# Optimization experiments

Hardware: AMD Instinct MI355X
Metric: run time of the kernel (lower is better)

The kernel has to match this reference:

```python
import jax, jax.numpy as jnp
import numpy as np
from jax import lax

HEADS = 4
SR = 4
LN_EPS = 1e-5


def setup_inputs() -> dict:
    key = jax.random.key(0)
    ks = jax.random.split(key, 8)
    B, N, C = 8, 4096, 256
    w_scale = 0.05  # keep attention logits in a sane range
    return {
        "x": jax.random.normal(ks[0], (B, N, C), jnp.float32),
        "h": 64,
        "w": 64,
        "Wq": jax.random.normal(ks[1], (C, C), jnp.float32) * w_scale,
        "Wkv": jax.random.normal(ks[2], (C, 2 * C), jnp.float32) * w_scale,
        "sr_w": jax.random.normal(ks[3], (C, C, SR, SR), jnp.float32) * w_scale,
        "sr_b": jnp.zeros((C,), jnp.float32),
        "ln_g": jnp.ones((C,), jnp.float32),
        "ln_b": jnp.zeros((C,), jnp.float32),
        "Wo": jax.random.normal(ks[4], (C, C), jnp.float32) * w_scale,
        "bo": jnp.zeros((C,), jnp.float32),
    }


def _layernorm(x, g, b):
    mu = x.mean(-1, keepdims=True)
    var = ((x - mu) ** 2).mean(-1, keepdims=True)
    return (x - mu) * lax.rsqrt(var + LN_EPS) * g + b


def reference(x, h, w, Wq, Wkv, sr_w, sr_b, ln_g, ln_b, Wo, bo):
    B, N, C = x.shape
    hd = C // HEADS
    scale = hd ** -0.5
    # Q projection -> [B, H, N, hd]
    q = (x @ Wq).reshape(B, N, HEADS, hd).transpose(0, 2, 1, 3)
    # spatial reduction of K/V tokens: strided conv + LayerNorm
    x_kv = x.transpose(0, 2, 1).reshape(B, C, h, w)  # b (h w) c -> b c h w
    x_kv = lax.conv_general_dilated(
        x_kv, sr_w, window_strides=(SR, SR), padding="VALID",
        dimension_numbers=("NCHW", "OIHW", "NCHW"))
    x_kv = x_kv + sr_b[None, :, None, None]
    Nk = (h // SR) * (w // SR)
    x_kv = x_kv.reshape(B, C, Nk).transpose(0, 2, 1)  # b c h w -> b (h w) c
    x_kv = _layernorm(x_kv, ln_g, ln_b)
    # KV projection -> k, v each [B, H, Nk, hd]
    kv = (x_kv @ Wkv).reshape(B, Nk, 2, HEADS, hd)
    k = kv[:, :, 0].transpose(0, 2, 1, 3)
    v = kv[:, :, 1].transpose(0, 2, 1, 3)
    # attention: full [B, H, N, Nk] score matrix, softmax over kv axis
    att = jax.nn.softmax(jnp.einsum("bhxd,bhyd->bhxy", q, k) * scale, axis=-1)
    out = jnp.einsum("bhxy,bhyd->bhxd", att, v)
    out = out.transpose(0, 2, 1, 3).reshape(B, N, C)  # b h l d -> b l (h d)
    return out @ Wo + bo
```

## Files before the change

kernel.cpp:

```cpp
#include <hip/hip_runtime.h>

typedef __bf16 bf16;
typedef bf16 bf16x8 __attribute__((ext_vector_type(8)));
typedef bf16 bf16x4 __attribute__((ext_vector_type(4)));
typedef float f32x4 __attribute__((ext_vector_type(4)));

#define MFMA16(a, b, c) __builtin_amdgcn_mfma_f32_16x16x32_bf16(a, b, c, 0, 0, 0)

__global__ void k_prep(const float* __restrict__ x, const float* __restrict__ Wq,
                       const float* __restrict__ Wkv, const float* __restrict__ Wo,
                       const float* __restrict__ srw,
                       bf16* __restrict__ x_bf, bf16* __restrict__ WqT,
                       bf16* __restrict__ WkvT, bf16* __restrict__ WoT,
                       bf16* __restrict__ srwT) {
  int bid = blockIdx.x, tid = threadIdx.x;
  if (bid < 8192) {
    int i = (bid * 256 + tid) * 4;
    float4 v = *(const float4*)(x + i);
    bf16x4 o;
    o[0] = (bf16)v.x; o[1] = (bf16)v.y; o[2] = (bf16)v.z; o[3] = (bf16)v.w;
    *(bf16x4*)(x_bf + i) = o;
  } else if (bid < 9216) {
    int id = (bid - 8192) * 256 + tid;
    if (id < 65536) {
      int c = id >> 8, r = id & 255;
      WqT[id] = (bf16)Wq[r * 256 + c];
    } else if (id < 196608) {
      int l = id - 65536;
      int c = l >> 8, r = l & 255;
      WkvT[l] = (bf16)Wkv[r * 512 + c];
    } else {
      int l = id - 196608;
      int c = l >> 8, r = l & 255;
      WoT[l] = (bf16)Wo[r * 256 + c];
    }
  } else {
    int id4 = ((bid - 9216) * 256 + tid) * 4;
    int o = id4 >> 12, rem = id4 & 4095;
    int i = rem >> 4, p = rem & 15;
    float4 v = *(const float4*)(srw + id4);
    srwT[(o << 12) + ((p + 0) << 8) + i] = (bf16)v.x;
    srwT[(o << 12) + ((p + 1) << 8) + i] = (bf16)v.y;
    srwT[(o << 12) + ((p + 2) << 8) + i] = (bf16)v.z;
    srwT[(o << 12) + ((p + 3) << 8) + i] = (bf16)v.w;
  }
}

template <int AMODE, int EMODE>
__global__ __launch_bounds__(256, 2) void k_gemm(
    const bf16* __restrict__ A, const bf16* __restrict__ Bt,
    void* __restrict__ Cout, const float* __restrict__ bias,
    int M, int N, int K) {
  constexpr int LDT = 72;
  __shared__ alignas(16) bf16 As[64 * LDT];
  __shared__ alignas(16) bf16 Bs[64 * LDT];
  int tid = threadIdx.x;
  int m0 = blockIdx.x * 64, n0 = blockIdx.y * 64;
  int kbeg = blockIdx.z * K;
  int wave = tid >> 6, lane = tid & 63;
  int quad = lane >> 4, l16 = lane & 15;

  f32x4 acc[4];
#pragma unroll
  for (int i = 0; i < 4; i++) acc[i] = (f32x4){0.f, 0.f, 0.f, 0.f};

  for (int k0 = kbeg; k0 < kbeg + K; k0 += 64) {
#pragma unroll
    for (int t = 0; t < 2; t++) {
      int c = tid + t * 256;
      int row = c >> 3, c8 = (c & 7) * 8;
      const bf16* asrc;
      if constexpr (AMODE == 0) {
        asrc = A + (size_t)(m0 + row) * K + k0 + c8;
      } else {
        int m = m0 + row;
        int b = m >> 8, tt = m & 255;
        int oh = tt >> 4, ow = tt & 15;
        int p = k0 >> 8;
        int kh = p >> 2, kw = p & 3;
        int tok = (oh * 4 + kh) * 64 + ow * 4 + kw;
        asrc = A + ((size_t)(b * 4096 + tok) << 8) + (k0 & 255) + c8;
      }
      *(bf16x8*)&As[row * LDT + c8] = *(const bf16x8*)asrc;
      *(bf16x8*)&Bs[row * LDT + c8] =
          *(const bf16x8*)(Bt + (size_t)(n0 + row) * ((AMODE == 1) ? 4096 : K) + k0 + c8);
    }
    __syncthreads();
#pragma unroll
    for (int kk = 0; kk < 64; kk += 32) {
      bf16x8 af = *(const bf16x8*)&As[(wave * 16 + l16) * LDT + kk + quad * 8];
#pragma unroll
      for (int nt = 0; nt < 4; nt++) {
        bf16x8 bfr = *(const bf16x8*)&Bs[(nt * 16 + l16) * LDT + kk + quad * 8];
        acc[nt] = MFMA16(af, bfr, acc[nt]);
      }
    }
    __syncthreads();
  }

  int rbase = m0 + wave * 16 + quad * 4;
#pragma unroll
  for (int nt = 0; nt < 4; nt++) {
    int col = n0 + nt * 16 + l16;
#pragma unroll
    for (int r = 0; r < 4; r++) {
      float v = acc[nt][r];
      int row = rbase + r;
      if constexpr (EMODE == 2) {
        int b = row >> 8, key = row & 255;
        int isv = col >> 8, c2 = col & 255;
        int hh = c2 >> 6, d = c2 & 63;
        int bh = b * 4 + hh;
        bf16* dst = (bf16*)Cout;
        if (isv == 0)
          dst[(((size_t)bh) * 256 + key) * 64 + d] = (bf16)v;
        else
          dst[32 * 256 * 64 + (((size_t)bh) * 64 + d) * 256 + key] = (bf16)v;
      } else if constexpr (EMODE == 3) {
        ((float*)Cout)[(size_t)row * N + col] = v + bias[col];
      } else {
        ((float*)Cout)[((size_t)blockIdx.z * M + row) * N + col] = v;
      }
    }
  }
}

__global__ void k_ln(const float* __restrict__ part, const float* __restrict__ srb,
                     const float* __restrict__ g, const float* __restrict__ bb,
                     bf16* __restrict__ out) {
  int row = blockIdx.x * 4 + (threadIdx.x >> 6);
  int lane = threadIdx.x & 63;
  size_t off = (size_t)row * 256 + lane * 4;
  float4 v = *(const float4*)&part[off];
#pragma unroll
  for (int z = 1; z < 8; z++) {
    float4 p = *(const float4*)&part[(size_t)z * 2048 * 256 + off];
    v.x += p.x; v.y += p.y; v.z += p.z; v.w += p.w;
  }
  int c = lane * 4;
  v.x += srb[c + 0]; v.y += srb[c + 1]; v.z += srb[c + 2]; v.w += srb[c + 3];
  float s = v.x + v.y + v.z + v.w;
#pragma unroll
  for (int i = 1; i < 64; i <<= 1) s += __shfl_xor(s, i, 64);
  float mu = s * (1.f / 256.f);
  float d0 = v.x - mu, d1 = v.y - mu, d2 = v.z - mu, d3 = v.w - mu;
  float q = d0 * d0 + d1 * d1 + d2 * d2 + d3 * d3;
#pragma unroll
  for (int i = 1; i < 64; i <<= 1) q += __shfl_xor(q, i, 64);
  float rs = rsqrtf(q * (1.f / 256.f) + 1e-5f);
  bf16x4 o;
  o[0] = (bf16)(d0 * rs * g[c + 0] + bb[c + 0]);
  o[1] = (bf16)(d1 * rs * g[c + 1] + bb[c + 1]);
  o[2] = (bf16)(d2 * rs * g[c + 2] + bb[c + 2]);
  o[3] = (bf16)(d3 * rs * g[c + 3] + bb[c + 3]);
  *(bf16x4*)&out[(size_t)row * 256 + c] = o;
}

__global__ __launch_bounds__(256, 2) void k_attn(
    const bf16* __restrict__ xbf,
    const bf16* __restrict__ WqT,
    const bf16* __restrict__ Kb,
    const bf16* __restrict__ Vt_g,
    bf16* __restrict__ O) {
  int bh = blockIdx.x, qt = blockIdx.y;
  int b = bh >> 2, h = bh & 3;
  int tid = threadIdx.x, wave = tid >> 6, lane = tid & 63;
  int quad = lane >> 4, l16 = lane & 15;

  __shared__ alignas(16) bf16 smem[39936];
  bf16* R1 = smem;
  bf16* R2 = smem + 18432;
  bf16* Qs = smem + 35328;

#pragma unroll
  for (int t = 0; t < 8; t++) {
    int c = tid + t * 256;
    int row = c >> 5, c8 = (c & 31) * 8;
    *(bf16x8*)&R1[row * 264 + c8] =
        *(const bf16x8*)&xbf[((size_t)(b * 4096 + qt * 64 + row) << 8) + c8];
    *(bf16x8*)&R2[row * 264 + c8] =
        *(const bf16x8*)&WqT[((size_t)(h * 64 + row) << 8) + c8];
  }
  __syncthreads();

  f32x4 q[4];
#pragma unroll
  for (int i = 0; i < 4; i++) q[i] = (f32x4){0.f, 0.f, 0.f, 0.f};
#pragma unroll
  for (int k0 = 0; k0 < 256; k0 += 32) {
    bf16x8 ax = *(const bf16x8*)&R1[(wave * 16 + l16) * 264 + k0 + quad * 8];
#pragma unroll
    for (int nt = 0; nt < 4; nt++) {
      bf16x8 bw = *(const bf16x8*)&R2[(nt * 16 + l16) * 264 + k0 + quad * 8];
      q[nt] = MFMA16(ax, bw, q[nt]);
    }
  }
  __syncthreads();

#pragma unroll
  for (int nt = 0; nt < 4; nt++)
#pragma unroll
    for (int r = 0; r < 4; r++)
      Qs[(wave * 16 + quad * 4 + r) * 72 + nt * 16 + l16] = (bf16)q[nt][r];

  const bf16* Kbh = Kb + (size_t)bh * 256 * 64;
#pragma unroll
  for (int t = 0; t < 8; t++) {
    int c = tid + t * 256;
    int row = c >> 3, c8 = (c & 7) * 8;
    *(bf16x8*)&R1[row * 72 + c8] = *(const bf16x8*)&Kbh[row * 64 + c8];
  }
  const bf16* Vbh = Vt_g + (size_t)bh * 64 * 256;
#pragma unroll
  for (int t = 0; t < 8; t++) {
    int c = tid + t * 256;
    int row = c >> 5, c8 = (c & 31) * 8;
    *(bf16x8*)&R2[row * 264 + c8] = *(const bf16x8*)&Vbh[row * 256 + c8];
  }
  __syncthreads();

  f32x4 s[16];
#pragma unroll
  for (int i = 0; i < 16; i++) s[i] = (f32x4){0.f, 0.f, 0.f, 0.f};
  bf16x8 aq0 = *(const bf16x8*)&Qs[(wave * 16 + l16) * 72 + 0 + quad * 8];
  bf16x8 aq1 = *(const bf16x8*)&Qs[(wave * 16 + l16) * 72 + 32 + quad * 8];
#pragma unroll
  for (int nt = 0; nt < 16; nt++) {
    bf16x8 b0 = *(const bf16x8*)&R1[(nt * 16 + l16) * 72 + 0 + quad * 8];
    bf16x8 b1 = *(const bf16x8*)&R1[(nt * 16 + l16) * 72 + 32 + quad * 8];
    s[nt] = MFMA16(aq0, b0, s[nt]);
    s[nt] = MFMA16(aq1, b1, s[nt]);
  }

  const float scale = 0.125f;
#pragma unroll
  for (int r = 0; r < 4; r++) {
    float m = -1e30f;
#pragma unroll
    for (int nt = 0; nt < 16; nt++) m = fmaxf(m, s[nt][r]);
#pragma unroll
    for (int i = 1; i < 16; i <<= 1) m = fmaxf(m, __shfl_xor(m, i, 64));
    float sum = 0.f;
#pragma unroll
    for (int nt = 0; nt < 16; nt++) {
      float e = __expf((s[nt][r] - m) * scale);
      s[nt][r] = e;
      sum += e;
    }
#pragma unroll
    for (int i = 1; i < 16; i <<= 1) sum += __shfl_xor(sum, i, 64);
    float inv = 1.f / sum;
#pragma unroll
    for (int nt = 0; nt < 16; nt++) s[nt][r] *= inv;
  }

  __syncthreads();
#pragma unroll
  for (int nt = 0; nt < 16; nt++)
#pragma unroll
    for (int r = 0; r < 4; r++)
      R1[(wave * 16 + quad * 4 + r) * 264 + nt * 16 + l16] = (bf16)s[nt][r];
  __syncthreads();

  f32x4 o[4];
#pragma unroll
  for (int i = 0; i < 4; i++) o[i] = (f32x4){0.f, 0.f, 0.f, 0.f};
#pragma unroll
  for (int k0 = 0; k0 < 256; k0 += 32) {
    bf16x8 ap = *(const bf16x8*)&R1[(wave * 16 + l16) * 264 + k0 + quad * 8];
#pragma unroll
    for (int nt = 0; nt < 4; nt++) {
      bf16x8 bv = *(const bf16x8*)&R2[(nt * 16 + l16) * 264 + k0 + quad * 8];
      o[nt] = MFMA16(ap, bv, o[nt]);
    }
  }

  size_t orow = (size_t)b * 4096 + qt * 64 + wave * 16 + quad * 4;
#pragma unroll
  for (int nt = 0; nt < 4; nt++) {
    int col = h * 64 + nt * 16 + l16;
#pragma unroll
    for (int r = 0; r < 4; r++) O[(orow + r) * 256 + col] = (bf16)o[nt][r];
  }
}

extern "C" void kernel_launch(void* const* d_in, const int* in_sizes, int n_in,
                              void* d_out, int out_size, void* d_ws, size_t ws_size,
                              hipStream_t stream) {
  (void)in_sizes; (void)n_in; (void)out_size; (void)ws_size;
  const float* x   = (const float*)d_in[0];
  const float* Wq  = (const float*)d_in[3];
  const float* Wkv = (const float*)d_in[4];
  const float* srw = (const float*)d_in[5];
  const float* srb = (const float*)d_in[6];
  const float* lng = (const float*)d_in[7];
  const float* lnb = (const float*)d_in[8];
  const float* Wo  = (const float*)d_in[9];
  const float* bo  = (const float*)d_in[10];
  float* out = (float*)d_out;

  char* ws = (char*)d_ws;
  bf16*  x_bf  = (bf16*)(ws + 0);
  bf16*  AObuf = (bf16*)(ws + 16777216);
  float* convp = (float*)(ws + 33554432);
  bf16*  WqT   = (bf16*)(ws + 50331648);
  bf16*  WkvT  = (bf16*)(ws + 50462720);
  bf16*  WoT   = (bf16*)(ws + 50724864);
  bf16*  srwT  = (bf16*)(ws + 50855936);
  bf16*  xln   = (bf16*)(ws + 52953088);
  bf16*  kvbuf = (bf16*)(ws + 54001664);

  k_prep<<<10240, 256, 0, stream>>>(x, Wq, Wkv, Wo, srw, x_bf, WqT, WkvT, WoT, srwT);
  k_gemm<1, 4><<<dim3(32, 4, 8), 256, 0, stream>>>(x_bf, srwT, convp, nullptr, 2048, 256, 512);
  k_ln<<<512, 256, 0, stream>>>(convp, srb, lng, lnb, xln);
  k_gemm<0, 2><<<dim3(32, 8), 256, 0, stream>>>(xln, WkvT, kvbuf, nullptr, 2048, 512, 256);
  k_attn<<<dim3(32, 64), 256, 0, stream>>>(x_bf, WqT, kvbuf, kvbuf + (size_t)32 * 256 * 64, AObuf);
  k_gemm<0, 3><<<dim3(512, 4), 256, 0, stream>>>(AObuf, WoT, out, bo, 32768, 256, 256);
}
```

Before: 189.3 us.

## Load attention MFMA operands directly from global memory instead of LDS staging

```diff
diff --git a/kernel.cpp b/kernel.cpp
--- a/kernel.cpp
+++ b/kernel.cpp
@@ -156,7 +156,7 @@
   *(bf16x4*)&out[(size_t)row * 256 + c] = o;
 }
 
-__global__ __launch_bounds__(256, 2) void k_attn(
+__global__ __launch_bounds__(256, 4) void k_attn(
     const bf16* __restrict__ xbf,
     const bf16* __restrict__ WqT,
     const bf16* __restrict__ Kb,
@@ -167,67 +167,41 @@
   int tid = threadIdx.x, wave = tid >> 6, lane = tid & 63;
   int quad = lane >> 4, l16 = lane & 15;
 
-  __shared__ alignas(16) bf16 smem[39936];
-  bf16* R1 = smem;
-  bf16* R2 = smem + 18432;
-  bf16* Qs = smem + 35328;
-
-#pragma unroll
-  for (int t = 0; t < 8; t++) {
-    int c = tid + t * 256;
-    int row = c >> 5, c8 = (c & 31) * 8;
-    *(bf16x8*)&R1[row * 264 + c8] =
-        *(const bf16x8*)&xbf[((size_t)(b * 4096 + qt * 64 + row) << 8) + c8];
-    *(bf16x8*)&R2[row * 264 + c8] =
-        *(const bf16x8*)&WqT[((size_t)(h * 64 + row) << 8) + c8];
-  }
-  __syncthreads();
-
+  __shared__ alignas(16) bf16 smem[64 * 264];
+
+  const bf16* xrow =
+      xbf + (((size_t)(b * 4096 + qt * 64 + wave * 16 + l16)) << 8) + quad * 8;
+  const bf16* wq = WqT + (((size_t)(h * 64)) << 8) + quad * 8;
   f32x4 q[4];
 #pragma unroll
   for (int i = 0; i < 4; i++) q[i] = (f32x4){0.f, 0.f, 0.f, 0.f};
 #pragma unroll
   for (int k0 = 0; k0 < 256; k0 += 32) {
-    bf16x8 ax = *(const bf16x8*)&R1[(wave * 16 + l16) * 264 + k0 + quad * 8];
+    bf16x8 ax = *(const bf16x8*)(xrow + k0);
 #pragma unroll
     for (int nt = 0; nt < 4; nt++) {
-      bf16x8 bw = *(const bf16x8*)&R2[(nt * 16 + l16) * 264 + k0 + quad * 8];
+      bf16x8 bw = *(const bf16x8*)(wq + ((nt * 16 + l16) << 8) + k0);
       q[nt] = MFMA16(ax, bw, q[nt]);
     }
   }
-  __syncthreads();
 
 #pragma unroll
   for (int nt = 0; nt < 4; nt++)
 #pragma unroll
     for (int r = 0; r < 4; r++)
-      Qs[(wave * 16 + quad * 4 + r) * 72 + nt * 16 + l16] = (bf16)q[nt][r];
-
-  const bf16* Kbh = Kb + (size_t)bh * 256 * 64;
-#pragma unroll
-  for (int t = 0; t < 8; t++) {
-    int c = tid + t * 256;
-    int row = c >> 3, c8 = (c & 7) * 8;
-    *(bf16x8*)&R1[row * 72 + c8] = *(const bf16x8*)&Kbh[row * 64 + c8];
-  }
-  const bf16* Vbh = Vt_g + (size_t)bh * 64 * 256;
-#pragma unroll
-  for (int t = 0; t < 8; t++) {
-    int c = tid + t * 256;
-    int row = c >> 5, c8 = (c & 31) * 8;
-    *(bf16x8*)&R2[row * 264 + c8] = *(const bf16x8*)&Vbh[row * 256 + c8];
-  }
-  __syncthreads();
-
+      smem[(wave * 16 + quad * 4 + r) * 72 + nt * 16 + l16] = (bf16)q[nt][r];
+
+  bf16x8 aq0 = *(const bf16x8*)&smem[(wave * 16 + l16) * 72 + 0 + quad * 8];
+  bf16x8 aq1 = *(const bf16x8*)&smem[(wave * 16 + l16) * 72 + 32 + quad * 8];
+
+  const bf16* Kbh = Kb + (((size_t)bh) << 14) + quad * 8;
   f32x4 s[16];
 #pragma unroll
   for (int i = 0; i < 16; i++) s[i] = (f32x4){0.f, 0.f, 0.f, 0.f};
-  bf16x8 aq0 = *(const bf16x8*)&Qs[(wave * 16 + l16) * 72 + 0 + quad * 8];
-  bf16x8 aq1 = *(const bf16x8*)&Qs[(wave * 16 + l16) * 72 + 32 + quad * 8];
 #pragma unroll
   for (int nt = 0; nt < 16; nt++) {
-    bf16x8 b0 = *(const bf16x8*)&R1[(nt * 16 + l16) * 72 + 0 + quad * 8];
-    bf16x8 b1 = *(const bf16x8*)&R1[(nt * 16 + l16) * 72 + 32 + quad * 8];
+    bf16x8 b0 = *(const bf16x8*)(Kbh + ((nt * 16 + l16) << 6));
+    bf16x8 b1 = *(const bf16x8*)(Kbh + ((nt * 16 + l16) << 6) + 32);
     s[nt] = MFMA16(aq0, b0, s[nt]);
     s[nt] = MFMA16(aq1, b1, s[nt]);
   }
@@ -259,18 +233,18 @@
   for (int nt = 0; nt < 16; nt++)
 #pragma unroll
     for (int r = 0; r < 4; r++)
-      R1[(wave * 16 + quad * 4 + r) * 264 + nt * 16 + l16] = (bf16)s[nt][r];
-  __syncthreads();
-
+      smem[(wave * 16 + quad * 4 + r) * 264 + nt * 16 + l16] = (bf16)s[nt][r];
+
+  const bf16* Vbh = Vt_g + (((size_t)bh) << 14) + quad * 8;
   f32x4 o[4];
 #pragma unroll
   for (int i = 0; i < 4; i++) o[i] = (f32x4){0.f, 0.f, 0.f, 0.f};
 #pragma unroll
   for (int k0 = 0; k0 < 256; k0 += 32) {
-    bf16x8 ap = *(const bf16x8*)&R1[(wave * 16 + l16) * 264 + k0 + quad * 8];
+    bf16x8 ap = *(const bf16x8*)&smem[(wave * 16 + l16) * 264 + k0 + quad * 8];
 #pragma unroll
     for (int nt = 0; nt < 4; nt++) {
-      bf16x8 bv = *(const bf16x8*)&R2[(nt * 16 + l16) * 264 + k0 + quad * 8];
+      bf16x8 bv = *(const bf16x8*)(Vbh + ((nt * 16 + l16) << 8) + k0);
       o[nt] = MFMA16(ap, bv, o[nt]);
     }
   }
```

New measurement: 244.0 us. 28.9% more time.
